# Kernel tuning notes

Measured on AMD Instinct MI355X. Metric: run time of the kernel, lower is better.

## Reference

```python
import jax, jax.numpy as jnp
import numpy as np

B, N, F, E, K, R, H = 16, 2048, 2048, 128, 10, 2, 2


def setup_inputs() -> dict:
    key = jax.random.key(0)
    ks = jax.random.split(key, 11)
    s = 0.1  # keep embeddings close so the Gaussian kernel does not underflow
    rel = jax.random.normal(ks[0], (B, E), jnp.float32) * s
    arg1 = jax.random.normal(ks[1], (B, E), jnp.float32) * s
    arg2 = jax.random.normal(ks[2], (B, E), jnp.float32) * s
    fact_rel = jax.random.normal(ks[3], (B, F, E), jnp.float32) * s
    fact_arg1 = jax.random.normal(ks[4], (B, F, E), jnp.float32) * s
    fact_arg2 = jax.random.normal(ks[5], (B, F, E), jnp.float32) * s
    entity_embeddings = jax.random.normal(ks[6], (B, N, E), jnp.float32) * s
    hop_W = jax.random.normal(ks[7], (R, H, E, E), jnp.float32) / jnp.sqrt(jnp.float32(E))
    hop_b = jax.random.normal(ks[8], (R, H, E), jnp.float32) * 0.01
    nb_facts = jax.random.randint(ks[9], (B,), F // 2, F + 1, jnp.int32)
    nb_entities = jax.random.randint(ks[10], (B,), N // 2, N + 1, jnp.int32)
    return dict(rel=rel, arg1=arg1, arg2=arg2, fact_rel=fact_rel,
                fact_arg1=fact_arg1, fact_arg2=fact_arg2,
                entity_embeddings=entity_embeddings, hop_W=hop_W, hop_b=hop_b,
                nb_facts=nb_facts, nb_entities=nb_entities)


def reference(rel, arg1, arg2, fact_rel, fact_arg1, fact_arg2,
              entity_embeddings, hop_W, hop_b, nb_facts, nb_entities):
    # Gaussian kernel k(x,y) = exp(-||x-y||^2 / 2), batched: x [B,T,E], y [B,F,E] -> [B,T,F]
    def kern(x, y):
        d2 = (jnp.sum(x * x, -1)[:, :, None] + jnp.sum(y * y, -1)[:, None, :]
              - 2.0 * jnp.einsum('bte,bfe->btf', x, y))
        return jnp.exp(-0.5 * d2)

    fact_mask = (jnp.arange(F) < nb_facts[:, None])[:, None, :]            # [B,1,F]
    ent_mask = (jnp.arange(N) < nb_entities[:, None]).astype(rel.dtype)    # [B,N]

    # BatchNeuralKB.score: max over (valid) facts of product of kernels. [B,T,E]x3 -> [B,T]
    def model_score(r, a1, a2):
        s = kern(r, fact_rel) * kern(a1, fact_arg1) * kern(a2, fact_arg2)  # [B,T,F]
        return jnp.max(jnp.where(fact_mask, s, 0.0), axis=-1)

    # BatchNeuralKB.forward, (s,p,?) -> score per candidate object entity. [B,1,E] -> [B,N]
    def forward_sp(r, a1):
        kr = jnp.where(fact_mask, kern(r, fact_rel) * kern(a1, fact_arg1), 0.0)  # [B,1,F]
        kE = kern(entity_embeddings, fact_arg2)                                  # [B,N,F]
        return jnp.max(kr * kE, axis=-1) * ent_mask                              # [B,N]

    # (?,p,o) -> score per candidate subject entity
    def forward_po(r, a2):
        kr = jnp.where(fact_mask, kern(r, fact_rel) * kern(a2, fact_arg2), 0.0)
        kE = kern(entity_embeddings, fact_arg1)
        return jnp.max(kr * kE, axis=-1) * ent_mask

    # r_score(depth=1) = max(depth_r_score(0), depth_r_score(1))
    # depth_r_score(0) == model.score
    scores_0 = model_score(rel[:, None], arg1[:, None], arg2[:, None])[:, 0]  # [B]

    global_res = None
    for r_idx in range(R):
        is_rev = (r_idx % 2 == 1)
        # LinearReformulator: hop relations from rel
        h1 = rel @ hop_W[r_idx, 0] + hop_b[r_idx, 0]  # [B,E]
        h2 = rel @ hop_W[r_idx, 1] + hop_b[r_idx, 1]
        # hop 1: r_hop -> scores over all entities, then top-k beam
        if is_rev:
            sp = forward_po(h1[:, None], arg1[:, None])  # [B,N]
        else:
            sp = forward_sp(h1[:, None], arg1[:, None])
        z_scores, z_idx = jax.lax.top_k(sp, K)                                  # [B,K]
        z_emb = jnp.take_along_axis(entity_embeddings, z_idx[:, :, None], axis=1)  # [B,K,E]
        # final hop: r_score(depth=0) == model.score with branched args
        h2k = jnp.broadcast_to(h2[:, None, :], (B, K, E))
        a2k = jnp.broadcast_to(arg2[:, None, :], (B, K, E))
        if is_rev:
            s2 = model_score(h2k, a2k, z_emb)  # [B,K]
        else:
            s2 = model_score(h2k, z_emb, a2k)
        rule_scores = jnp.minimum(s2, z_scores)   # tnorm = 'min'
        rule_res = jnp.max(rule_scores, axis=1)   # max over branches [B]
        global_res = rule_res if global_res is None else jnp.maximum(global_res, rule_res)

    return jnp.maximum(scores_0, global_res)
```

## Files before the change

kernel.cpp:

```cpp
#include <hip/hip_runtime.h>
#include <math.h>

#define Bb 16
#define Nn 2048
#define Ff 2048
#define Ee 128
#define Kk 10
#define S2FC 8
#define S2F (Ff / S2FC)

typedef __attribute__((ext_vector_type(8))) short short8;
typedef __attribute__((ext_vector_type(4))) float f32x4;

__device__ inline float wave_sum(float x) {
    for (int o = 32; o; o >>= 1) x += __shfl_down(x, o);
    return x;
}

__device__ inline void bsplit(float x, unsigned short& h, unsigned short& l) {
    unsigned int u = __float_as_uint(x);
    h = (unsigned short)(u >> 16);
    float hf = __uint_as_float(u & 0xFFFF0000u);
    l = (unsigned short)(__float_as_uint(x - hf) >> 16);
}

__global__ __launch_bounds__(256) void k_bsplit(
    const float* __restrict__ fa1, const float* __restrict__ fa2,
    unsigned short* __restrict__ B0, unsigned short* __restrict__ B1) {
    int g = blockIdx.x * 256 + threadIdx.x;
    const float* src = (blockIdx.y == 0) ? fa2 : fa1;
    unsigned short* dst = ((blockIdx.y == 0) ? B0 : B1) + (size_t)g * 16;
    int f = g & 2047, oct = (g >> 11) & 15, b = g >> 15;
    const float* s = src + ((size_t)b * Ff + f) * Ee + oct * 8;
    float4 v0 = *(const float4*)s;
    float4 v1 = *(const float4*)(s + 4);
    float xs[8] = {v0.x, v0.y, v0.z, v0.w, v1.x, v1.y, v1.z, v1.w};
    unsigned short hi[8], lo[8];
#pragma unroll
    for (int j = 0; j < 8; ++j) bsplit(xs[j], hi[j], lo[j]);
    uint4 ph, pl;
    ph.x = (unsigned)hi[0] | ((unsigned)hi[1] << 16);
    ph.y = (unsigned)hi[2] | ((unsigned)hi[3] << 16);
    ph.z = (unsigned)hi[4] | ((unsigned)hi[5] << 16);
    ph.w = (unsigned)hi[6] | ((unsigned)hi[7] << 16);
    pl.x = (unsigned)lo[0] | ((unsigned)lo[1] << 16);
    pl.y = (unsigned)lo[2] | ((unsigned)lo[3] << 16);
    pl.z = (unsigned)lo[4] | ((unsigned)lo[5] << 16);
    pl.w = (unsigned)lo[6] | ((unsigned)lo[7] << 16);
    *(uint4*)dst = ph;
    *(uint4*)(dst + 8) = pl;
}

__global__ void k_hops(const float* __restrict__ rel, const float* __restrict__ hop_W,
                       const float* __restrict__ hop_b, float* __restrict__ h) {
    int rj = blockIdx.x;
    int b  = blockIdx.y;
    int e  = threadIdx.x;
    const float* W  = hop_W + (size_t)rj * Ee * Ee;
    const float* rb = rel + b * Ee;
    float acc = hop_b[rj * Ee + e];
    for (int i = 0; i < Ee; ++i) acc += rb[i] * W[i * Ee + e];
    h[((size_t)rj * Bb + b) * Ee + e] = acc;
}

__global__ void k_entnorm(const float* __restrict__ ent, float* __restrict__ ent_norm) {
    int row  = blockIdx.x * 4 + (threadIdx.x >> 6);
    int lane = threadIdx.x & 63;
    const float* p = ent + (size_t)row * Ee;
    float a = p[lane], c = p[lane + 64];
    float s = wave_sum(a * a + c * c);
    if (lane == 0) ent_norm[row] = s;
}

__global__ void k_facts(const float* __restrict__ rel, const float* __restrict__ arg1,
                        const float* __restrict__ arg2, const float* __restrict__ frel,
                        const float* __restrict__ fa1, const float* __restrict__ fa2,
                        const float* __restrict__ h, const int* __restrict__ nb_facts,
                        float* __restrict__ c0, float* __restrict__ c1,
                        float* __restrict__ s2b0, float* __restrict__ s2b1,
                        float* __restrict__ lsc0) {
    int f = blockIdx.x, b = blockIdx.y;
    int lane = threadIdx.x;
    size_t fb = ((size_t)b * Ff + f) * Ee;
    float d_rr = 0, d_a11 = 0, d_a22 = 0, d_h10 = 0, d_h11 = 0, d_h20 = 0, d_h21 = 0;
    float d_a12 = 0, d_a21 = 0, n1 = 0, n2 = 0;
#pragma unroll
    for (int half = 0; half < 2; ++half) {
        int e = lane + half * 64;
        float vr = frel[fb + e], v1 = fa1[fb + e], v2 = fa2[fb + e];
        float qr = rel[b * Ee + e], q1 = arg1[b * Ee + e], q2 = arg2[b * Ee + e];
        float h10 = h[((size_t)0 * Bb + b) * Ee + e];
        float h20 = h[((size_t)1 * Bb + b) * Ee + e];
        float h11 = h[((size_t)2 * Bb + b) * Ee + e];
        float h21 = h[((size_t)3 * Bb + b) * Ee + e];
        float t;
        t = qr - vr;  d_rr  += t * t;
        t = q1 - v1;  d_a11 += t * t;
        t = q2 - v2;  d_a22 += t * t;
        t = h10 - vr; d_h10 += t * t;
        t = h11 - vr; d_h11 += t * t;
        t = h20 - vr; d_h20 += t * t;
        t = h21 - vr; d_h21 += t * t;
        t = q1 - v2;  d_a12 += t * t;
        t = q2 - v1;  d_a21 += t * t;
        n1 += v1 * v1; n2 += v2 * v2;
    }
    d_rr = wave_sum(d_rr);   d_a11 = wave_sum(d_a11); d_a22 = wave_sum(d_a22);
    d_h10 = wave_sum(d_h10); d_h11 = wave_sum(d_h11); d_h20 = wave_sum(d_h20);
    d_h21 = wave_sum(d_h21); d_a12 = wave_sum(d_a12); d_a21 = wave_sum(d_a21);
    n1 = wave_sum(n1);       n2 = wave_sum(n2);
    if (lane == 0) {
        bool valid = f < nb_facts[b];
        const float NI = -INFINITY;
        size_t o = (size_t)b * Ff + f;
        lsc0[o] = valid ? -0.5f * (d_rr + d_a11 + d_a22) : NI;
        c0[o]   = valid ? (-0.5f * (d_h10 + d_a11 + n2)) : NI;
        c1[o]   = valid ? (-0.5f * (d_h11 + d_a12 + n1)) : NI;
        s2b0[o] = valid ? (-0.5f * (d_h20 + d_a22)) : NI;
        s2b1[o] = valid ? (-0.5f * (d_h21 + d_a21)) : NI;
    }
}

#define BMs 128

__global__ __launch_bounds__(256, 2) void k_spmax_mfma(
    const float* __restrict__ ent, const unsigned short* __restrict__ B0,
    const unsigned short* __restrict__ B1, const float* __restrict__ c0,
    const float* __restrict__ c1, const float* __restrict__ ent_norm,
    const int* __restrict__ nb_entities, float* __restrict__ sp0,
    float* __restrict__ sp1) {
    int nblk = blockIdx.x, b = blockIdx.y, r = blockIdx.z;
    const unsigned short* Bt = (r == 0) ? B0 : B1;
    const float* cb = ((r == 0) ? c0 : c1) + (size_t)b * Ff;
    float* sp = ((r == 0) ? sp0 : sp1) + (size_t)b * Nn;

    int tid = threadIdx.x;
    int wave = tid >> 6, lane = tid & 63;
    int wm = wave >> 1, wn = wave & 1;
    int lane15 = lane & 15, quad = lane >> 4;

    short8 ah[4][4], al[4][4];
    {
        const float* abase = ent + ((size_t)b * Nn + (size_t)nblk * BMs + wm * 64) * Ee;
#pragma unroll
        for (int i = 0; i < 4; ++i)
#pragma unroll
            for (int ks = 0; ks < 4; ++ks) {
                const float* p = abase + (size_t)(i * 16 + lane15) * Ee + ks * 32 + quad * 8;
                float4 v0 = *(const float4*)p;
                float4 v1 = *(const float4*)(p + 4);
                float xs[8] = {v0.x, v0.y, v0.z, v0.w, v1.x, v1.y, v1.z, v1.w};
#pragma unroll
                for (int j = 0; j < 8; ++j) {
                    unsigned short hh, ll;
                    bsplit(xs[j], hh, ll);
                    ah[i][ks][j] = (short)hh;
                    al[i][ks][j] = (short)ll;
                }
            }
    }

    const unsigned short* bbase =
        Bt + ((((size_t)b * 16 + quad) * Ff) + wn * 32 + lane15) * 16;

    float mmax[4][4];
#pragma unroll
    for (int i = 0; i < 4; ++i)
#pragma unroll
        for (int rr = 0; rr < 4; ++rr) mmax[i][rr] = -INFINITY;

    for (int f0 = 0; f0 < Ff; f0 += 64) {
        f32x4 acc[4][2];
#pragma unroll
        for (int i = 0; i < 4; ++i)
#pragma unroll
            for (int j = 0; j < 2; ++j) acc[i][j] = (f32x4){0.f, 0.f, 0.f, 0.f};

#pragma unroll
        for (int ks = 0; ks < 4; ++ks) {
            const unsigned short* p0 = bbase + (size_t)ks * 4 * Ff * 16 + (size_t)f0 * 16;
            const unsigned short* p1 = p0 + 16 * 16;
            short8 bh0 = *(const short8*)p0;
            short8 bl0 = *(const short8*)(p0 + 8);
            short8 bh1 = *(const short8*)p1;
            short8 bl1 = *(const short8*)(p1 + 8);
#pragma unroll
            for (int i = 0; i < 4; ++i) {
                acc[i][0] = __builtin_amdgcn_mfma_f32_16x16x32_bf16(ah[i][ks], bh0, acc[i][0], 0, 0, 0);
                acc[i][0] = __builtin_amdgcn_mfma_f32_16x16x32_bf16(al[i][ks], bh0, acc[i][0], 0, 0, 0);
                acc[i][0] = __builtin_amdgcn_mfma_f32_16x16x32_bf16(ah[i][ks], bl0, acc[i][0], 0, 0, 0);
                acc[i][1] = __builtin_amdgcn_mfma_f32_16x16x32_bf16(ah[i][ks], bh1, acc[i][1], 0, 0, 0);
                acc[i][1] = __builtin_amdgcn_mfma_f32_16x16x32_bf16(al[i][ks], bh1, acc[i][1], 0, 0, 0);
                acc[i][1] = __builtin_amdgcn_mfma_f32_16x16x32_bf16(ah[i][ks], bl1, acc[i][1], 0, 0, 0);
            }
        }

#pragma unroll
        for (int j = 0; j < 2; ++j) {
            float cj = cb[f0 + wn * 32 + j * 16 + lane15];
#pragma unroll
            for (int i = 0; i < 4; ++i)
#pragma unroll
                for (int rr = 0; rr < 4; ++rr)
                    mmax[i][rr] = fmaxf(mmax[i][rr], acc[i][j][rr] + cj);
        }
    }

    __shared__ float red[BMs][2];
#pragma unroll
    for (int i = 0; i < 4; ++i)
#pragma unroll
        for (int rr = 0; rr < 4; ++rr) {
            float v = mmax[i][rr];
#pragma unroll
            for (int m = 1; m < 16; m <<= 1) v = fmaxf(v, __shfl_xor(v, m));
            if (lane15 == 0) red[wm * 64 + i * 16 + quad * 4 + rr][wn] = v;
        }
    __syncthreads();
    if (tid < BMs) {
        float m = fmaxf(red[tid][0], red[tid][1]);
        int n = nblk * BMs + tid;
        float v = (n < nb_entities[b]) ? expf(m - 0.5f * ent_norm[(size_t)b * Nn + n]) : 0.0f;
        sp[n] = v;
    }
}

__global__ void k_topk(const float* __restrict__ sp0, const float* __restrict__ sp1,
                       float* __restrict__ z_scores, int* __restrict__ z_idx) {
    int b = blockIdx.x, r = blockIdx.y;
    const float* sp = ((r == 0) ? sp0 : sp1) + (size_t)b * Nn;
    __shared__ float vals[Nn];
    __shared__ float bv[256];
    __shared__ int   bi[256];
    int tid = threadIdx.x;
    for (int i = tid; i < Nn; i += 256) vals[i] = sp[i];
    __syncthreads();
    for (int k = 0; k < Kk; ++k) {
        float best = -1.0f; int bidx = Nn;
        for (int i = tid; i < Nn; i += 256) {
            float v = vals[i];
            if (v > best) { best = v; bidx = i; }
        }
        bv[tid] = best; bi[tid] = bidx;
        __syncthreads();
        for (int s = 128; s > 0; s >>= 1) {
            if (tid < s) {
                float v2 = bv[tid + s]; int i2 = bi[tid + s];
                if (v2 > bv[tid] || (v2 == bv[tid] && i2 < bi[tid])) { bv[tid] = v2; bi[tid] = i2; }
            }
            __syncthreads();
        }
        if (tid == 0) {
            z_scores[((size_t)b * 2 + r) * Kk + k] = bv[0];
            z_idx[((size_t)b * 2 + r) * Kk + k]    = bi[0];
            vals[bi[0]] = -1.0f;
        }
        __syncthreads();
    }
}

__global__ __launch_bounds__(256) void k_s2(
    const float* __restrict__ ent, const float* __restrict__ fa1,
    const float* __restrict__ fa2, const float* __restrict__ s2b0,
    const float* __restrict__ s2b1, const int* __restrict__ z_idx,
    float* __restrict__ partial ) {
    int fc = blockIdx.x, b = blockIdx.y, r = blockIdx.z;
    const float* factX = (r == 0) ? fa1 : fa2;
    const float* s2b   = ((r == 0) ? s2b0 : s2b1) + (size_t)b * Ff;

    __shared__ float zsh[Kk][Ee];
    __shared__ float znorm[Kk];
    __shared__ int   zish[Kk];
    __shared__ float red[4][Kk];

    int tid = threadIdx.x;
    if (tid < Kk) zish[tid] = z_idx[((size_t)b * 2 + r) * Kk + tid];
    __syncthreads();
    for (int idx = tid; idx < Kk * Ee; idx += 256) {
        int k = idx >> 7, e = idx & 127;
        zsh[k][e] = ent[((size_t)b * Nn + zish[k]) * Ee + e];
    }
    __syncthreads();
    if (tid < Kk) {
        float s = 0.f;
        for (int e = 0; e < Ee; ++e) { float v = zsh[tid][e]; s += v * v; }
        znorm[tid] = s;
    }
    __syncthreads();

    int f = fc * S2F + tid;
    const float* fp = factX + ((size_t)b * Ff + f) * Ee;
    float acc[Kk];
#pragma unroll
    for (int k = 0; k < Kk; ++k) acc[k] = 0.f;
    float nf = 0.f;
#pragma unroll 4
    for (int e0 = 0; e0 < Ee; e0 += 4) {
        float4 v = *(const float4*)(fp + e0);
        nf += v.x * v.x + v.y * v.y + v.z * v.z + v.w * v.w;
#pragma unroll
        for (int k = 0; k < Kk; ++k) {
            float4 z = *(const float4*)&zsh[k][e0];
            acc[k] += z.x * v.x + z.y * v.y + z.z * v.z + z.w * v.w;
        }
    }
    float base = s2b[f] - 0.5f * nf;
    float sc[Kk];
#pragma unroll
    for (int k = 0; k < Kk; ++k) sc[k] = base + acc[k] - 0.5f * znorm[k];
    for (int o = 32; o; o >>= 1)
#pragma unroll
        for (int k = 0; k < Kk; ++k) sc[k] = fmaxf(sc[k], __shfl_down(sc[k], o));
    int wv = tid >> 6;
    if ((tid & 63) == 0)
#pragma unroll
        for (int k = 0; k < Kk; ++k) red[wv][k] = sc[k];
    __syncthreads();
    if (tid < Kk) {
        float m = fmaxf(fmaxf(red[0][tid], red[1][tid]), fmaxf(red[2][tid], red[3][tid]));
        partial[(((size_t)b * 2 + r) * S2FC + fc) * Kk + tid] = m;
    }
}

__global__ void k_final(const float* __restrict__ lsc0, const float* __restrict__ partial,
                        const float* __restrict__ z_scores, float* __restrict__ out) {
    int b = blockIdx.x, tid = threadIdx.x;
    __shared__ float sm[256];
    float m = -INFINITY;
    for (int f = tid; f < Ff; f += 256) m = fmaxf(m, lsc0[(size_t)b * Ff + f]);
    sm[tid] = m;
    __syncthreads();
    for (int s = 128; s > 0; s >>= 1) {
        if (tid < s) sm[tid] = fmaxf(sm[tid], sm[tid + s]);
        __syncthreads();
    }
    if (tid == 0) {
        float sc0 = expf(sm[0]);
        float g = -INFINITY;
        for (int r = 0; r < 2; ++r)
            for (int k = 0; k < Kk; ++k) {
                float mm = -INFINITY;
                for (int fc = 0; fc < S2FC; ++fc)
                    mm = fmaxf(mm, partial[(((size_t)b * 2 + r) * S2FC + fc) * Kk + k]);
                float rule = fminf(expf(mm), z_scores[((size_t)b * 2 + r) * Kk + k]);
                g = fmaxf(g, rule);
            }
        out[b] = fmaxf(sc0, g);
    }
}

extern "C" void kernel_launch(void* const* d_in, const int* in_sizes, int n_in,
                              void* d_out, int out_size, void* d_ws, size_t ws_size,
                              hipStream_t stream) {
    const float* rel  = (const float*)d_in[0];
    const float* arg1 = (const float*)d_in[1];
    const float* arg2 = (const float*)d_in[2];
    const float* frel = (const float*)d_in[3];
    const float* fa1  = (const float*)d_in[4];
    const float* fa2  = (const float*)d_in[5];
    const float* ent  = (const float*)d_in[6];
    const float* hopW = (const float*)d_in[7];
    const float* hopb = (const float*)d_in[8];
    const int* nb_facts    = (const int*)d_in[9];
    const int* nb_entities = (const int*)d_in[10];
    float* out = (float*)d_out;

    float* ws = (float*)d_ws;
    size_t off = 0;
    float* h        = ws + off; off += 4 * Bb * Ee;
    float* c0       = ws + off; off += (size_t)Bb * Ff;
    float* c1       = ws + off; off += (size_t)Bb * Ff;
    float* s2b0     = ws + off; off += (size_t)Bb * Ff;
    float* s2b1     = ws + off; off += (size_t)Bb * Ff;
    float* lsc0     = ws + off; off += (size_t)Bb * Ff;
    float* sp0      = ws + off; off += (size_t)Bb * Nn;
    float* sp1      = ws + off; off += (size_t)Bb * Nn;
    float* ent_norm = ws + off; off += (size_t)Bb * Nn;
    float* z_scores = ws + off; off += Bb * 2 * Kk;
    float* partial  = ws + off; off += (size_t)Bb * 2 * S2FC * Kk;
    int*   z_idx    = (int*)(ws + off); off += Bb * 2 * Kk;
    off = (off + 7) & ~(size_t)7;
    unsigned short* B0 = (unsigned short*)(ws + off); off += (size_t)Bb * 16 * Ff * 8;
    unsigned short* B1 = (unsigned short*)(ws + off); off += (size_t)Bb * 16 * Ff * 8;

    k_bsplit<<<dim3(Bb * 16 * Ff / 256, 2), 256, 0, stream>>>(fa1, fa2, B0, B1);
    k_hops<<<dim3(4, Bb), 128, 0, stream>>>(rel, hopW, hopb, h);
    k_entnorm<<<dim3(Bb * Nn / 4), 256, 0, stream>>>(ent, ent_norm);
    k_facts<<<dim3(Ff, Bb), 64, 0, stream>>>(rel, arg1, arg2, frel, fa1, fa2, h,
                                             nb_facts, c0, c1, s2b0, s2b1, lsc0);
    k_spmax_mfma<<<dim3(Nn / BMs, Bb, 2), 256, 0, stream>>>(ent, B0, B1, c0, c1, ent_norm,
                                                            nb_entities, sp0, sp1);
    k_topk<<<dim3(Bb, 2), 256, 0, stream>>>(sp0, sp1, z_scores, z_idx);
    k_s2<<<dim3(S2FC, Bb, 2), 256, 0, stream>>>(ent, fa1, fa2, s2b0, s2b1, z_idx, partial);
    k_final<<<dim3(Bb), 256, 0, stream>>>(lsc0, partial, z_scores, out);
}
```

Measured before the change: 271.6 us.

## Move A low parts to LDS, prefetch B, fold bias, wave-level top-k

The MFMA scoring kernel now keeps only the bf16 high halves of the entity tile in registers and stages the low halves in shared memory, which cuts register pressure. It also software-prefetches the next B fragments, seeds the accumulators with the per-fact bias instead of adding it afterwards, and reuses the LDS buffer for the final reduction. The bsplit kernel is remapped so neighbouring threads read contiguous fact rows, and top-k becomes a single-wave register and shuffle reduction with no block barriers. The risks are extra LDS reads inside the inner loop and higher register use from holding prefetched fragments.

```diff
diff --git a/kernel.cpp b/kernel.cpp
--- a/kernel.cpp
+++ b/kernel.cpp
@@ -27,10 +27,13 @@
 __global__ __launch_bounds__(256) void k_bsplit(
     const float* __restrict__ fa1, const float* __restrict__ fa2,
     unsigned short* __restrict__ B0, unsigned short* __restrict__ B1) {
-    int g = blockIdx.x * 256 + threadIdx.x;
+    int tid = threadIdx.x;
+    int oct = tid & 15, fl = tid >> 4;
+    int bx = blockIdx.x;
+    int b = bx >> 7, f = (bx & 127) * 16 + fl;
     const float* src = (blockIdx.y == 0) ? fa2 : fa1;
-    unsigned short* dst = ((blockIdx.y == 0) ? B0 : B1) + (size_t)g * 16;
-    int f = g & 2047, oct = (g >> 11) & 15, b = g >> 15;
+    unsigned short* dst = ((blockIdx.y == 0) ? B0 : B1) +
+                          (((size_t)b * 16 + oct) * Ff + f) * 16;
     const float* s = src + ((size_t)b * Ff + f) * Ee + oct * 8;
     float4 v0 = *(const float4*)s;
     float4 v1 = *(const float4*)(s + 4);
@@ -134,12 +137,14 @@
     const float* cb = ((r == 0) ? c0 : c1) + (size_t)b * Ff;
     float* sp = ((r == 0) ? sp0 : sp1) + (size_t)b * Nn;
 
+    __shared__ unsigned short alds[2 * 4 * 4 * 64 * 8];
+
     int tid = threadIdx.x;
     int wave = tid >> 6, lane = tid & 63;
     int wm = wave >> 1, wn = wave & 1;
     int lane15 = lane & 15, quad = lane >> 4;
 
-    short8 ah[4][4], al[4][4];
+    short8 ah[4][4];
     {
         const float* abase = ent + ((size_t)b * Nn + (size_t)nblk * BMs + wm * 64) * Ee;
 #pragma unroll
@@ -150,63 +155,87 @@
                 float4 v0 = *(const float4*)p;
                 float4 v1 = *(const float4*)(p + 4);
                 float xs[8] = {v0.x, v0.y, v0.z, v0.w, v1.x, v1.y, v1.z, v1.w};
+                short8 hi8, lo8;
 #pragma unroll
                 for (int j = 0; j < 8; ++j) {
                     unsigned short hh, ll;
                     bsplit(xs[j], hh, ll);
-                    ah[i][ks][j] = (short)hh;
-                    al[i][ks][j] = (short)ll;
+                    hi8[j] = (short)hh;
+                    lo8[j] = (short)ll;
                 }
+                ah[i][ks] = hi8;
+                if (wn == 0)
+                    *(short8*)&alds[(((wm * 4 + i) * 4 + ks) * 64 + lane) * 8] = lo8;
             }
     }
+    __syncthreads();
 
     const unsigned short* bbase =
         Bt + ((((size_t)b * 16 + quad) * Ff) + wn * 32 + lane15) * 16;
 
+    short8 pbh0[4], pbl0[4], pbh1[4], pbl1[4];
+#pragma unroll
+    for (int ks = 0; ks < 4; ++ks) {
+        const unsigned short* p0 = bbase + ((size_t)ks * 4 * Ff) * 16;
+        pbh0[ks] = *(const short8*)p0;
+        pbl0[ks] = *(const short8*)(p0 + 8);
+        pbh1[ks] = *(const short8*)(p0 + 256);
+        pbl1[ks] = *(const short8*)(p0 + 264);
+    }
+
     float mmax[4][4];
 #pragma unroll
     for (int i = 0; i < 4; ++i)
 #pragma unroll
         for (int rr = 0; rr < 4; ++rr) mmax[i][rr] = -INFINITY;
 
-    for (int f0 = 0; f0 < Ff; f0 += 64) {
+    for (int c = 0; c < 32; ++c) {
+        int f0 = c * 64;
+        float cj0 = cb[f0 + wn * 32 + lane15];
+        float cj1 = cb[f0 + wn * 32 + 16 + lane15];
         f32x4 acc[4][2];
 #pragma unroll
-        for (int i = 0; i < 4; ++i)
-#pragma unroll
-            for (int j = 0; j < 2; ++j) acc[i][j] = (f32x4){0.f, 0.f, 0.f, 0.f};
+        for (int i = 0; i < 4; ++i) {
+            acc[i][0] = (f32x4){cj0, cj0, cj0, cj0};
+            acc[i][1] = (f32x4){cj1, cj1, cj1, cj1};
+        }
+        int fn = ((c + 1) & 31) * 64;
 
 #pragma unroll
         for (int ks = 0; ks < 4; ++ks) {
-            const unsigned short* p0 = bbase + (size_t)ks * 4 * Ff * 16 + (size_t)f0 * 16;
-            const unsigned short* p1 = p0 + 16 * 16;
-            short8 bh0 = *(const short8*)p0;
-            short8 bl0 = *(const short8*)(p0 + 8);
-            short8 bh1 = *(const short8*)p1;
-            short8 bl1 = *(const short8*)(p1 + 8);
+            short8 bh0 = pbh0[ks], bl0 = pbl0[ks], bh1 = pbh1[ks], bl1 = pbl1[ks];
+            const unsigned short* p0 = bbase + ((size_t)ks * 4 * Ff + fn) * 16;
+            pbh0[ks] = *(const short8*)p0;
+            pbl0[ks] = *(const short8*)(p0 + 8);
+            pbh1[ks] = *(const short8*)(p0 + 256);
+            pbl1[ks] = *(const short8*)(p0 + 264);
+            short8 al0 = *(short8*)&alds[(((wm * 4 + 0) * 4 + ks) * 64 + lane) * 8];
+            short8 al1 = *(short8*)&alds[(((wm * 4 + 1) * 4 + ks) * 64 + lane) * 8];
+            short8 al2 = *(short8*)&alds[(((wm * 4 + 2) * 4 + ks) * 64 + lane) * 8];
+            short8 al3 = *(short8*)&alds[(((wm * 4 + 3) * 4 + ks) * 64 + lane) * 8];
+            short8 alv[4] = {al0, al1, al2, al3};
 #pragma unroll
             for (int i = 0; i < 4; ++i) {
                 acc[i][0] = __builtin_amdgcn_mfma_f32_16x16x32_bf16(ah[i][ks], bh0, acc[i][0], 0, 0, 0);
-                acc[i][0] = __builtin_amdgcn_mfma_f32_16x16x32_bf16(al[i][ks], bh0, acc[i][0], 0, 0, 0);
+                acc[i][0] = __builtin_amdgcn_mfma_f32_16x16x32_bf16(alv[i],    bh0, acc[i][0], 0, 0, 0);
                 acc[i][0] = __builtin_amdgcn_mfma_f32_16x16x32_bf16(ah[i][ks], bl0, acc[i][0], 0, 0, 0);
                 acc[i][1] = __builtin_amdgcn_mfma_f32_16x16x32_bf16(ah[i][ks], bh1, acc[i][1], 0, 0, 0);
-                acc[i][1] = __builtin_amdgcn_mfma_f32_16x16x32_bf16(al[i][ks], bh1, acc[i][1], 0, 0, 0);
+                acc[i][1] = __builtin_amdgcn_mfma_f32_16x16x32_bf16(alv[i],    bh1, acc[i][1], 0, 0, 0);
                 acc[i][1] = __builtin_amdgcn_mfma_f32_16x16x32_bf16(ah[i][ks], bl1, acc[i][1], 0, 0, 0);
             }
         }
 
 #pragma unroll
-        for (int j = 0; j < 2; ++j) {
-            float cj = cb[f0 + wn * 32 + j * 16 + lane15];
+        for (int j = 0; j < 2; ++j)
 #pragma unroll
             for (int i = 0; i < 4; ++i)
 #pragma unroll
                 for (int rr = 0; rr < 4; ++rr)
-                    mmax[i][rr] = fmaxf(mmax[i][rr], acc[i][j][rr] + cj);
-        }
-    }
-
-    __shared__ float red[BMs][2];
+                    mmax[i][rr] = fmaxf(mmax[i][rr], acc[i][j][rr]);
+    }
+
+    __syncthreads();
+    float* red = (float*)alds;
 #pragma unroll
     for (int i = 0; i < 4; ++i)
 #pragma unroll
@@ -214,11 +243,11 @@
             float v = mmax[i][rr];
 #pragma unroll
             for (int m = 1; m < 16; m <<= 1) v = fmaxf(v, __shfl_xor(v, m));
-            if (lane15 == 0) red[wm * 64 + i * 16 + quad * 4 + rr][wn] = v;
+            if (lane15 == 0) red[(wm * 64 + i * 16 + quad * 4 + rr) * 2 + wn] = v;
         }
     __syncthreads();
     if (tid < BMs) {
-        float m = fmaxf(red[tid][0], red[tid][1]);
+        float m = fmaxf(red[tid * 2], red[tid * 2 + 1]);
         int n = nblk * BMs + tid;
         float v = (n < nb_entities[b]) ? expf(m - 0.5f * ent_norm[(size_t)b * Nn + n]) : 0.0f;
         sp[n] = v;
@@ -229,33 +258,31 @@
                        float* __restrict__ z_scores, int* __restrict__ z_idx) {
     int b = blockIdx.x, r = blockIdx.y;
     const float* sp = ((r == 0) ? sp0 : sp1) + (size_t)b * Nn;
-    __shared__ float vals[Nn];
-    __shared__ float bv[256];
-    __shared__ int   bi[256];
-    int tid = threadIdx.x;
-    for (int i = tid; i < Nn; i += 256) vals[i] = sp[i];
-    __syncthreads();
+    int lane = threadIdx.x;
+    float v[Nn / 64];
+#pragma unroll
+    for (int i = 0; i < Nn / 64; ++i) v[i] = sp[i * 64 + lane];
     for (int k = 0; k < Kk; ++k) {
-        float best = -1.0f; int bidx = Nn;
-        for (int i = tid; i < Nn; i += 256) {
-            float v = vals[i];
-            if (v > best) { best = v; bidx = i; }
-        }
-        bv[tid] = best; bi[tid] = bidx;
-        __syncthreads();
-        for (int s = 128; s > 0; s >>= 1) {
-            if (tid < s) {
-                float v2 = bv[tid + s]; int i2 = bi[tid + s];
-                if (v2 > bv[tid] || (v2 == bv[tid] && i2 < bi[tid])) { bv[tid] = v2; bi[tid] = i2; }
-            }
-            __syncthreads();
-        }
-        if (tid == 0) {
-            z_scores[((size_t)b * 2 + r) * Kk + k] = bv[0];
-            z_idx[((size_t)b * 2 + r) * Kk + k]    = bi[0];
-            vals[bi[0]] = -1.0f;
-        }
-        __syncthreads();
+        float best = -INFINITY; int bidx = 0;
+#pragma unroll
+        for (int i = 0; i < Nn / 64; ++i)
+            if (v[i] > best) { best = v[i]; bidx = i * 64 + lane; }
+#pragma unroll
+        for (int m = 1; m < 64; m <<= 1) {
+            float ov = __shfl_xor(best, m);
+            int oi = __shfl_xor(bidx, m);
+            if (ov > best || (ov == best && oi < bidx)) { best = ov; bidx = oi; }
+        }
+        if (lane == 0) {
+            z_scores[((size_t)b * 2 + r) * Kk + k] = best;
+            z_idx[((size_t)b * 2 + r) * Kk + k]    = bidx;
+        }
+        if ((bidx & 63) == lane) {
+            int slot = bidx >> 6;
+#pragma unroll
+            for (int i = 0; i < Nn / 64; ++i)
+                if (i == slot) v[i] = -INFINITY;
+        }
     }
 }
 
@@ -383,14 +410,14 @@
     unsigned short* B0 = (unsigned short*)(ws + off); off += (size_t)Bb * 16 * Ff * 8;
     unsigned short* B1 = (unsigned short*)(ws + off); off += (size_t)Bb * 16 * Ff * 8;
 
-    k_bsplit<<<dim3(Bb * 16 * Ff / 256, 2), 256, 0, stream>>>(fa1, fa2, B0, B1);
+    k_bsplit<<<dim3(Bb * Ff / 16, 2), 256, 0, stream>>>(fa1, fa2, B0, B1);
     k_hops<<<dim3(4, Bb), 128, 0, stream>>>(rel, hopW, hopb, h);
     k_entnorm<<<dim3(Bb * Nn / 4), 256, 0, stream>>>(ent, ent_norm);
     k_facts<<<dim3(Ff, Bb), 64, 0, stream>>>(rel, arg1, arg2, frel, fa1, fa2, h,
                                              nb_facts, c0, c1, s2b0, s2b1, lsc0);
     k_spmax_mfma<<<dim3(Nn / BMs, Bb, 2), 256, 0, stream>>>(ent, B0, B1, c0, c1, ent_norm,
                                                             nb_entities, sp0, sp1);
-    k_topk<<<dim3(Bb, 2), 256, 0, stream>>>(sp0, sp1, z_scores, z_idx);
+    k_topk<<<dim3(Bb, 2), 64, 0, stream>>>(sp0, sp1, z_scores, z_idx);
     k_s2<<<dim3(S2FC, Bb, 2), 256, 0, stream>>>(ent, fa1, fa2, s2b0, s2b1, z_idx, partial);
     k_final<<<dim3(Bb), 256, 0, stream>>>(lsc0, partial, z_scores, out);
 }
```

Result: faster. 264.3 us (-2.7%).
